# Optimization experiments

Measured on AMD Instinct MI355X. Metric: run time of the kernel, lower is better.

## Reference

```python
import jax, jax.numpy as jnp
import numpy as np

B, N, C = 4, 2048, 768
H = 12
HD = C // H

def setup_inputs() -> dict:
    key = jax.random.key(0)
    k1, k2, k3, k4, k5 = jax.random.split(key, 5)
    x = jax.random.normal(k1, (B, N, C), dtype=jnp.float32)
    qkv_w = jax.random.normal(k2, (3 * C, C), dtype=jnp.float32) * (1.0 / np.sqrt(C))
    qkv_b = jax.random.normal(k3, (3 * C,), dtype=jnp.float32) * 0.02
    proj_w = jax.random.normal(k4, (C, C), dtype=jnp.float32) * (1.0 / np.sqrt(C))
    proj_b = jax.random.normal(k5, (C,), dtype=jnp.float32) * 0.02
    return {"x": x, "qkv_w": qkv_w, "qkv_b": qkv_b, "proj_w": proj_w, "proj_b": proj_b}

def reference(x, qkv_w, qkv_b, proj_w, proj_b):
    scale = HD ** (-0.5)
    # qkv projection: (B,N,3C)
    qkv = x @ qkv_w.T + qkv_b
    qkv = qkv.reshape(B, N, 3, H, HD).transpose(2, 0, 3, 1, 4)  # (3,B,H,N,HD)
    q, k, v = qkv[0], qkv[1], qkv[2]
    attn = jnp.einsum('bhqd,bhkd->bhqk', q, k) * scale  # (B,H,N,N)
    mask_value = -jnp.finfo(attn.dtype).max
    causal_mask = jnp.triu(jnp.ones((N, N), dtype=bool), k=1)
    attn = jnp.where(causal_mask, mask_value, attn)
    attn = jax.nn.softmax(attn, axis=-1)
    out = jnp.einsum('bhqk,bhkd->bhqd', attn, v)  # (B,H,N,HD)
    out = out.transpose(0, 2, 1, 3).reshape(B, N, C)
    return out @ proj_w.T + proj_b
```

## Files before the change

### kernel.cpp

```cpp
#include <hip/hip_runtime.h>
#include <hip/hip_bf16.h>


typedef __attribute__((ext_vector_type(8))) short bf16x8;
typedef __attribute__((ext_vector_type(4))) float f32x4;
typedef __attribute__((ext_vector_type(16))) float f32x16;

typedef __attribute__((address_space(3))) unsigned int lds_uint;
typedef __attribute__((address_space(1))) const unsigned int gbl_uint;

__device__ __forceinline__ void gload16(const void* g, void* l) {
  __builtin_amdgcn_global_load_lds((gbl_uint*)g, (lds_uint*)l, 16, 0, 0);
}

__device__ __forceinline__ unsigned short f2bf(float f) {
  unsigned u = __float_as_uint(f);
  unsigned rounding = 0x7FFFu + ((u >> 16) & 1u);
  return (unsigned short)((u + rounding) >> 16);
}

__device__ __forceinline__ unsigned cvtpk(float lo, float hi) {
  unsigned r;
  asm("v_cvt_pk_bf16_f32 %0, %1, %2" : "=v"(r) : "v"(lo), "v"(hi));
  return r;
}

__device__ __forceinline__ float exp2a(float x) {
  float r;
  asm("v_exp_f32 %0, %1" : "=v"(r) : "v"(x));
  return r;
}

__global__ void cast_f32_to_bf16(const float* __restrict__ in,
                                 unsigned short* __restrict__ out, int n) {
  int idx = blockIdx.x * blockDim.x + threadIdx.x;
  int stride = gridDim.x * blockDim.x;
  for (int i = idx * 4; i < n; i += stride * 4) {
    float4 v = *reinterpret_cast<const float4*>(in + i);
    ushort4 o;
    o.x = f2bf(v.x); o.y = f2bf(v.y); o.z = f2bf(v.z); o.w = f2bf(v.w);
    *reinterpret_cast<ushort4*>(out + i) = o;
  }
}

template <bool OUT_F32>
__global__ __launch_bounds__(256) void gemm_bt_kernel(
    const unsigned short* __restrict__ A,
    const unsigned short* __restrict__ Bw,
    const float* __restrict__ bias,
    void* __restrict__ Cout,
    int M, int Ncols, int K, int ldc) {
  __shared__ __align__(16) short As[2][4096];
  __shared__ __align__(16) short Bs[2][4096];

  const int t = threadIdx.x;
  const int lane = t & 63;
  const int wave = t >> 6;
  const int wm = wave >> 1;
  const int wn = wave & 1;
  const int m0 = blockIdx.y * 128;
  const int n0 = blockIdx.x * 128;
  const int lrow = lane & 15;
  const int lk = (lane >> 4) * 8;

  const int srow = t >> 2, scol = (t & 3) * 8;
  const unsigned short* gA0 = A + (size_t)(m0 + srow) * K + scol;
  const unsigned short* gA1 = gA0 + (size_t)64 * K;
  const unsigned short* gB0 = Bw + (size_t)(n0 + srow) * K + scol;
  const unsigned short* gB1 = gB0 + (size_t)64 * K;
  const int db0 = wave * 512, db1 = 2048 + wave * 512;

  f32x4 acc[4][4] = {};
  const int nk = K / 32;

  gload16(gA0, &As[0][db0]); gload16(gA1, &As[0][db1]);
  gload16(gB0, &Bs[0][db0]); gload16(gB1, &Bs[0][db1]);

  int cur = 0;
  for (int kk = 0; kk < nk; ++kk) {
    __syncthreads();
    if (kk + 1 < nk) {
      const int off = (kk + 1) * 32;
      gload16(gA0 + off, &As[cur ^ 1][db0]); gload16(gA1 + off, &As[cur ^ 1][db1]);
      gload16(gB0 + off, &Bs[cur ^ 1][db0]); gload16(gB1 + off, &Bs[cur ^ 1][db1]);
    }
    bf16x8 a[4], b[4];
#pragma unroll
    for (int m = 0; m < 4; ++m)
      a[m] = *reinterpret_cast<const bf16x8*>(&As[cur][(wm * 64 + m * 16 + lrow) * 32 + lk]);
#pragma unroll
    for (int n = 0; n < 4; ++n)
      b[n] = *reinterpret_cast<const bf16x8*>(&Bs[cur][(wn * 64 + n * 16 + lrow) * 32 + lk]);
#pragma unroll
    for (int m = 0; m < 4; ++m)
#pragma unroll
      for (int n = 0; n < 4; ++n)
        acc[m][n] = __builtin_amdgcn_mfma_f32_16x16x32_bf16(a[m], b[n], acc[m][n], 0, 0, 0);
    cur ^= 1;
  }

  const int orow0 = (lane >> 4) * 4;
  const int ocol = lane & 15;
#pragma unroll
  for (int m = 0; m < 4; ++m) {
#pragma unroll
    for (int n = 0; n < 4; ++n) {
      const int c = n0 + wn * 64 + n * 16 + ocol;
      const float bv = bias[c];
#pragma unroll
      for (int r = 0; r < 4; ++r) {
        const int rr = m0 + wm * 64 + m * 16 + orow0 + r;
        const float v = acc[m][n][r] + bv;
        if (OUT_F32)
          reinterpret_cast<float*>(Cout)[(size_t)rr * ldc + c] = v;
        else
          reinterpret_cast<unsigned short*>(Cout)[(size_t)rr * ldc + c] = f2bf(v);
      }
    }
  }
}

#define ATT_N 2048
#define ATT_H 12
#define QKV_LD 2304

__global__ __launch_bounds__(256) void transpose_v(
    const unsigned short* __restrict__ qkv, unsigned short* __restrict__ vt) {
  const int kb = blockIdx.x;
  const int bh = blockIdx.y;
  const int t = threadIdx.x;
  const int b = bh / ATT_H, h = bh % ATT_H;
  const int d0 = (t & 7) * 8;
  const unsigned short* src = qkv + (size_t)(b * ATT_N) * QKV_LD + 1536 + h * 64 + d0;
  unsigned short* dst = vt + (size_t)bh * 64 * ATT_N + kb * 256;
#pragma unroll
  for (int kk = 0; kk < 8; ++kk) {
    const int ko = (t >> 3) + kk * 32;
    bf16x8 v = *reinterpret_cast<const bf16x8*>(src + (size_t)(kb * 256 + ko) * QKV_LD);
#pragma unroll
    for (int j = 0; j < 8; ++j)
      dst[(size_t)(d0 + j) * ATT_N + ko] = v[j];
  }
}

__global__ __launch_bounds__(256) void attn_kernel(
    const unsigned short* __restrict__ qkv,
    const unsigned short* __restrict__ vt,
    unsigned short* __restrict__ out) {
  __shared__ __align__(16) short Ks[2][4096];
  __shared__ __align__(16) short Vs[2][4096];

  const int t = threadIdx.x;
  const int lane = t & 63;
  const int w = t >> 6;
  const int hi = lane >> 5;
  const int l31 = lane & 31;

  const int wid = blockIdx.x;
  const int pj = wid / 48;
  const int bh = wid % 48;
  const int b = bh / ATT_H;
  const int h = bh % ATT_H;

  const size_t rowbase = (size_t)b * ATT_N;
  const unsigned short* qptr = qkv + rowbase * QKV_LD + h * 64;
  const unsigned short* kptr = qptr + 768;
  const unsigned short* vtptr = vt + (size_t)bh * 64 * ATT_N;

  int kKr[2], kKc[2];
#pragma unroll
  for (int c = 0; c < 2; ++c) {
    const int i = t + c * 256;
    const int f = i >> 6, ls = i & 63;
    kKr[c] = (f >> 2) * 32 + (ls & 31);
    kKc[c] = (f & 3) * 2 + (ls >> 5);
  }
  const unsigned short* gK0 = kptr + (size_t)kKr[0] * QKV_LD + kKc[0] * 8;
  const unsigned short* gK1 = kptr + (size_t)kKr[1] * QKV_LD + kKc[1] * 8;
  const unsigned short* gV0 = vtptr + (size_t)kKr[0] * ATT_N + kKc[0] * 8;
  const unsigned short* gV1 = vtptr + (size_t)kKr[1] * ATT_N + kKc[1] * 8;
  const int db0 = w * 512, db1 = 2048 + w * 512;

  for (int ph = 0; ph < 2; ++ph) {
    const int qb = ph ? pj : 15 - pj;
    const int q0w = qb * 128 + w * 32;
    const int qg = q0w + l31;
    const int nt = (qb + 1) * 2;

    bf16x8 qf[4];
#pragma unroll
    for (int dk = 0; dk < 4; ++dk)
      qf[dk] = *reinterpret_cast<const bf16x8*>(
          qptr + (size_t)(q0w + l31) * QKV_LD + dk * 16 + hi * 8);

    f32x16 O0 = {}, O1 = {};
    float lrun = 0.f;

    __syncthreads();
    gload16(gK0, &Ks[0][db0]); gload16(gK1, &Ks[0][db1]);
    gload16(gV0, &Vs[0][db0]); gload16(gV1, &Vs[0][db1]);

    int cur = 0;
    for (int kt = 0; kt < nt; ++kt) {
      const int k0 = kt * 64;
      __syncthreads();
      if (kt + 1 < nt) {
        const size_t advk = (size_t)(k0 + 64) * QKV_LD;
        gload16(gK0 + advk, &Ks[cur ^ 1][db0]); gload16(gK1 + advk, &Ks[cur ^ 1][db1]);
        gload16(gV0 + (k0 + 64), &Vs[cur ^ 1][db0]);
        gload16(gV1 + (k0 + 64), &Vs[cur ^ 1][db1]);
      }

      if (k0 <= q0w + 31) {
        f32x16 S0 = {}, S1 = {};
        __builtin_amdgcn_s_setprio(1);
#pragma unroll
        for (int dk = 0; dk < 4; ++dk) {
          bf16x8 kf = *reinterpret_cast<const bf16x8*>(&Ks[cur][(dk * 64 + lane) * 8]);
          S0 = __builtin_amdgcn_mfma_f32_32x32x16_bf16(kf, qf[dk], S0, 0, 0, 0);
        }
#pragma unroll
        for (int dk = 0; dk < 4; ++dk) {
          bf16x8 kf = *reinterpret_cast<const bf16x8*>(&Ks[cur][((4 + dk) * 64 + lane) * 8]);
          S1 = __builtin_amdgcn_mfma_f32_32x32x16_bf16(kf, qf[dk], S1, 0, 0, 0);
        }
        __builtin_amdgcn_s_setprio(0);

        const float scale2 = 0.18033688f;
        float p0[16], p1[16];
        if (k0 + 63 <= q0w) {
#pragma unroll
          for (int r = 0; r < 16; ++r) {
            p0[r] = exp2a(S0[r] * scale2);
            p1[r] = exp2a(S1[r] * scale2);
          }
        } else {
#pragma unroll
          for (int r = 0; r < 16; ++r) {
            int row = (r & 3) + 8 * (r >> 2) + 4 * hi;
            float e0 = (k0 + row > qg) ? -1e30f : S0[r] * scale2;
            float e1 = (k0 + 32 + row > qg) ? -1e30f : S1[r] * scale2;
            p0[r] = exp2a(e0);
            p1[r] = exp2a(e1);
          }
        }

        float sa = 0.f, sb = 0.f;
#pragma unroll
        for (int r = 0; r < 16; r += 2) { sa += p0[r] + p1[r]; sb += p0[r + 1] + p1[r + 1]; }
        float rsum = sa + sb;
        rsum += __shfl_xor(rsum, 32);
        lrun += rsum;

        bf16x8 Ub[4];
#pragma unroll
        for (int s = 0; s < 2; ++s) {
          unsigned pu[4][2];
#pragma unroll
          for (int m = 0; m < 4; ++m)
#pragma unroll
            for (int c = 0; c < 2; ++c)
              pu[m][c] = s ? cvtpk(p1[4 * m + 2 * c], p1[4 * m + 2 * c + 1])
                           : cvtpk(p0[4 * m + 2 * c], p0[4 * m + 2 * c + 1]);
#pragma unroll
          for (int tt = 0; tt < 2; ++tt) {
            unsigned s0v = hi ? pu[2 * tt][0] : pu[2 * tt + 1][0];
            unsigned s1v = hi ? pu[2 * tt][1] : pu[2 * tt + 1][1];
            unsigned r0 = __shfl_xor(s0v, 32);
            unsigned r1 = __shfl_xor(s1v, 32);
            union { unsigned u[4]; bf16x8 v; } U;
            U.u[0] = hi ? r0 : pu[2 * tt][0];
            U.u[1] = hi ? r1 : pu[2 * tt][1];
            U.u[2] = hi ? pu[2 * tt + 1][0] : r0;
            U.u[3] = hi ? pu[2 * tt + 1][1] : r1;
            Ub[s * 2 + tt] = U.v;
          }
        }

        __builtin_amdgcn_s_setprio(1);
#pragma unroll
        for (int ks = 0; ks < 4; ++ks) {
          bf16x8 vf0 = *reinterpret_cast<const bf16x8*>(&Vs[cur][(ks * 64 + lane) * 8]);
          O0 = __builtin_amdgcn_mfma_f32_32x32x16_bf16(vf0, Ub[ks], O0, 0, 0, 0);
          bf16x8 vf1 = *reinterpret_cast<const bf16x8*>(&Vs[cur][((4 + ks) * 64 + lane) * 8]);
          O1 = __builtin_amdgcn_mfma_f32_32x32x16_bf16(vf1, Ub[ks], O1, 0, 0, 0);
        }
        __builtin_amdgcn_s_setprio(0);
      }
      cur ^= 1;
    }

    const float inv = 1.0f / lrun;
    unsigned short* orow = out + (rowbase + q0w + l31) * 768 + h * 64;
#pragma unroll
    for (int half = 0; half < 2; ++half) {
      const f32x16& O = half ? O1 : O0;
#pragma unroll
      for (int m = 0; m < 4; ++m) {
        uint2 o2;
        o2.x = cvtpk(O[4 * m + 0] * inv, O[4 * m + 1] * inv);
        o2.y = cvtpk(O[4 * m + 2] * inv, O[4 * m + 3] * inv);
        *reinterpret_cast<uint2*>(orow + half * 32 + 8 * m + 4 * hi) = o2;
      }
    }
  }
}

extern "C" void kernel_launch(void* const* d_in, const int* in_sizes, int n_in,
                              void* d_out, int out_size, void* d_ws, size_t ws_size,
                              hipStream_t stream) {
  const float* x = (const float*)d_in[0];
  const float* qkv_w = (const float*)d_in[1];
  const float* qkv_b = (const float*)d_in[2];
  const float* proj_w = (const float*)d_in[3];
  const float* proj_b = (const float*)d_in[4];
  float* out = (float*)d_out;

  unsigned short* x_bf = (unsigned short*)d_ws;
  unsigned short* qw_bf = x_bf + (size_t)8192 * 768;
  unsigned short* pw_bf = qw_bf + (size_t)2304 * 768;
  unsigned short* qkv = pw_bf + (size_t)768 * 768;
  unsigned short* attno = qkv + (size_t)8192 * 2304;
  unsigned short* vtb = attno + (size_t)8192 * 768;

  cast_f32_to_bf16<<<dim3(1024), dim3(256), 0, stream>>>(x, x_bf, 8192 * 768);
  cast_f32_to_bf16<<<dim3(512), dim3(256), 0, stream>>>(qkv_w, qw_bf, 2304 * 768);
  cast_f32_to_bf16<<<dim3(256), dim3(256), 0, stream>>>(proj_w, pw_bf, 768 * 768);

  gemm_bt_kernel<false><<<dim3(18, 64), dim3(256), 0, stream>>>(
      x_bf, qw_bf, qkv_b, qkv, 8192, 2304, 768, 2304);
  transpose_v<<<dim3(8, 48), dim3(256), 0, stream>>>(qkv, vtb);
  attn_kernel<<<dim3(384), dim3(256), 0, stream>>>(qkv, vtb, attno);
  gemm_bt_kernel<true><<<dim3(6, 64), dim3(256), 0, stream>>>(
      attno, pw_bf, proj_b, out, 8192, 768, 768, 768);
}
```

Before: 163.8 us.

## Give each wave 64 query rows and drop the paired causal-block schedule

Each wave now handles 64 query rows in two 32-row groups instead of 32, so every K and V fragment read from LDS feeds two MFMAs. Work blocks become 256-query tiles processed largest-first (qb = 7 - wid/48), replacing the earlier scheme where each block handled two 128-row tiles paired for load balance. This roughly halves LDS traffic per unit of compute. In exchange it uses more registers (four accumulators, double the Q fragments), which can lower occupancy. Causal work per block is now uneven, and whether the grid launch was updated to match the new block count is not visible in the code shown.

```diff
diff --git a/kernel.cpp b/kernel.cpp
--- a/kernel.cpp
+++ b/kernel.cpp
@@ -157,7 +157,7 @@
   const int l31 = lane & 31;
 
   const int wid = blockIdx.x;
-  const int pj = wid / 48;
+  const int qb = 7 - (wid / 48);
   const int bh = wid % 48;
   const int b = bh / ATT_H;
   const int h = bh % ATT_H;
@@ -166,6 +166,21 @@
   const unsigned short* qptr = qkv + rowbase * QKV_LD + h * 64;
   const unsigned short* kptr = qptr + 768;
   const unsigned short* vtptr = vt + (size_t)bh * 64 * ATT_N;
+
+  const int q0w = qb * 256 + w * 64;
+  const int nt = (qb + 1) * 4;
+
+  bf16x8 qf0[4], qf1[4];
+#pragma unroll
+  for (int dk = 0; dk < 4; ++dk) {
+    qf0[dk] = *reinterpret_cast<const bf16x8*>(
+        qptr + (size_t)(q0w + l31) * QKV_LD + dk * 16 + hi * 8);
+    qf1[dk] = *reinterpret_cast<const bf16x8*>(
+        qptr + (size_t)(q0w + 32 + l31) * QKV_LD + dk * 16 + hi * 8);
+  }
+
+  f32x16 O00 = {}, O01 = {}, O10 = {}, O11 = {};
+  float lrun0 = 0.f, lrun1 = 0.f;
 
   int kKr[2], kKc[2];
 #pragma unroll
@@ -181,87 +196,72 @@
   const unsigned short* gV1 = vtptr + (size_t)kKr[1] * ATT_N + kKc[1] * 8;
   const int db0 = w * 512, db1 = 2048 + w * 512;
 
-  for (int ph = 0; ph < 2; ++ph) {
-    const int qb = ph ? pj : 15 - pj;
-    const int q0w = qb * 128 + w * 32;
-    const int qg = q0w + l31;
-    const int nt = (qb + 1) * 2;
-
-    bf16x8 qf[4];
-#pragma unroll
-    for (int dk = 0; dk < 4; ++dk)
-      qf[dk] = *reinterpret_cast<const bf16x8*>(
-          qptr + (size_t)(q0w + l31) * QKV_LD + dk * 16 + hi * 8);
-
-    f32x16 O0 = {}, O1 = {};
-    float lrun = 0.f;
-
+  gload16(gK0, &Ks[0][db0]); gload16(gK1, &Ks[0][db1]);
+  gload16(gV0, &Vs[0][db0]); gload16(gV1, &Vs[0][db1]);
+
+  int cur = 0;
+  for (int kt = 0; kt < nt; ++kt) {
+    const int k0 = kt * 64;
     __syncthreads();
-    gload16(gK0, &Ks[0][db0]); gload16(gK1, &Ks[0][db1]);
-    gload16(gV0, &Vs[0][db0]); gload16(gV1, &Vs[0][db1]);
-
-    int cur = 0;
-    for (int kt = 0; kt < nt; ++kt) {
-      const int k0 = kt * 64;
-      __syncthreads();
-      if (kt + 1 < nt) {
-        const size_t advk = (size_t)(k0 + 64) * QKV_LD;
-        gload16(gK0 + advk, &Ks[cur ^ 1][db0]); gload16(gK1 + advk, &Ks[cur ^ 1][db1]);
-        gload16(gV0 + (k0 + 64), &Vs[cur ^ 1][db0]);
-        gload16(gV1 + (k0 + 64), &Vs[cur ^ 1][db1]);
-      }
-
-      if (k0 <= q0w + 31) {
+    if (kt + 1 < nt) {
+      const size_t advk = (size_t)(k0 + 64) * QKV_LD;
+      gload16(gK0 + advk, &Ks[cur ^ 1][db0]); gload16(gK1 + advk, &Ks[cur ^ 1][db1]);
+      gload16(gV0 + (k0 + 64), &Vs[cur ^ 1][db0]);
+      gload16(gV1 + (k0 + 64), &Vs[cur ^ 1][db1]);
+    }
+
+    if (k0 <= q0w + 63) {
+#pragma unroll
+      for (int kh = 0; kh < 2; ++kh) {
+        const int kbase = k0 + kh * 32;
+        if (kbase > q0w + 63) break;
+
         f32x16 S0 = {}, S1 = {};
         __builtin_amdgcn_s_setprio(1);
 #pragma unroll
         for (int dk = 0; dk < 4; ++dk) {
-          bf16x8 kf = *reinterpret_cast<const bf16x8*>(&Ks[cur][(dk * 64 + lane) * 8]);
-          S0 = __builtin_amdgcn_mfma_f32_32x32x16_bf16(kf, qf[dk], S0, 0, 0, 0);
-        }
-#pragma unroll
-        for (int dk = 0; dk < 4; ++dk) {
-          bf16x8 kf = *reinterpret_cast<const bf16x8*>(&Ks[cur][((4 + dk) * 64 + lane) * 8]);
-          S1 = __builtin_amdgcn_mfma_f32_32x32x16_bf16(kf, qf[dk], S1, 0, 0, 0);
+          bf16x8 kf = *reinterpret_cast<const bf16x8*>(
+              &Ks[cur][((kh * 4 + dk) * 64 + lane) * 8]);
+          S0 = __builtin_amdgcn_mfma_f32_32x32x16_bf16(kf, qf0[dk], S0, 0, 0, 0);
+          S1 = __builtin_amdgcn_mfma_f32_32x32x16_bf16(kf, qf1[dk], S1, 0, 0, 0);
         }
         __builtin_amdgcn_s_setprio(0);
 
         const float scale2 = 0.18033688f;
         float p0[16], p1[16];
-        if (k0 + 63 <= q0w) {
+        if (kbase + 31 <= q0w) {
 #pragma unroll
           for (int r = 0; r < 16; ++r) {
             p0[r] = exp2a(S0[r] * scale2);
             p1[r] = exp2a(S1[r] * scale2);
           }
         } else {
+          const int qg0 = q0w + l31, qg1 = q0w + 32 + l31;
 #pragma unroll
           for (int r = 0; r < 16; ++r) {
-            int row = (r & 3) + 8 * (r >> 2) + 4 * hi;
-            float e0 = (k0 + row > qg) ? -1e30f : S0[r] * scale2;
-            float e1 = (k0 + 32 + row > qg) ? -1e30f : S1[r] * scale2;
-            p0[r] = exp2a(e0);
-            p1[r] = exp2a(e1);
+            const int key = kbase + (r & 3) + 8 * (r >> 2) + 4 * hi;
+            p0[r] = exp2a((key > qg0) ? -1e30f : S0[r] * scale2);
+            p1[r] = exp2a((key > qg1) ? -1e30f : S1[r] * scale2);
           }
         }
 
-        float sa = 0.f, sb = 0.f;
-#pragma unroll
-        for (int r = 0; r < 16; r += 2) { sa += p0[r] + p1[r]; sb += p0[r + 1] + p1[r + 1]; }
-        float rsum = sa + sb;
-        rsum += __shfl_xor(rsum, 32);
-        lrun += rsum;
-
-        bf16x8 Ub[4];
-#pragma unroll
-        for (int s = 0; s < 2; ++s) {
+        float ra = 0.f, rb = 0.f;
+#pragma unroll
+        for (int r = 0; r < 16; ++r) { ra += p0[r]; rb += p1[r]; }
+        ra += __shfl_xor(ra, 32);
+        rb += __shfl_xor(rb, 32);
+        lrun0 += ra; lrun1 += rb;
+
+        bf16x8 Ub0[2], Ub1[2];
+#pragma unroll
+        for (int g = 0; g < 2; ++g) {
+          const float* p = g ? p1 : p0;
           unsigned pu[4][2];
 #pragma unroll
           for (int m = 0; m < 4; ++m)
 #pragma unroll
             for (int c = 0; c < 2; ++c)
-              pu[m][c] = s ? cvtpk(p1[4 * m + 2 * c], p1[4 * m + 2 * c + 1])
-                           : cvtpk(p0[4 * m + 2 * c], p0[4 * m + 2 * c + 1]);
+              pu[m][c] = cvtpk(p[4 * m + 2 * c], p[4 * m + 2 * c + 1]);
 #pragma unroll
           for (int tt = 0; tt < 2; ++tt) {
             unsigned s0v = hi ? pu[2 * tt][0] : pu[2 * tt + 1][0];
@@ -273,34 +273,40 @@
             U.u[1] = hi ? r1 : pu[2 * tt][1];
             U.u[2] = hi ? pu[2 * tt + 1][0] : r0;
             U.u[3] = hi ? pu[2 * tt + 1][1] : r1;
-            Ub[s * 2 + tt] = U.v;
+            if (g == 0) Ub0[tt] = U.v; else Ub1[tt] = U.v;
           }
         }
 
         __builtin_amdgcn_s_setprio(1);
 #pragma unroll
-        for (int ks = 0; ks < 4; ++ks) {
+        for (int tt = 0; tt < 2; ++tt) {
+          const int ks = kh * 2 + tt;
           bf16x8 vf0 = *reinterpret_cast<const bf16x8*>(&Vs[cur][(ks * 64 + lane) * 8]);
-          O0 = __builtin_amdgcn_mfma_f32_32x32x16_bf16(vf0, Ub[ks], O0, 0, 0, 0);
+          O00 = __builtin_amdgcn_mfma_f32_32x32x16_bf16(vf0, Ub0[tt], O00, 0, 0, 0);
+          O01 = __builtin_amdgcn_mfma_f32_32x32x16_bf16(vf0, Ub1[tt], O01, 0, 0, 0);
           bf16x8 vf1 = *reinterpret_cast<const bf16x8*>(&Vs[cur][((4 + ks) * 64 + lane) * 8]);
-          O1 = __builtin_amdgcn_mfma_f32_32x32x16_bf16(vf1, Ub[ks], O1, 0, 0, 0);
+          O10 = __builtin_amdgcn_mfma_f32_32x32x16_bf16(vf1, Ub0[tt], O10, 0, 0, 0);
+          O11 = __builtin_amdgcn_mfma_f32_32x32x16_bf16(vf1, Ub1[tt], O11, 0, 0, 0);
         }
         __builtin_amdgcn_s_setprio(0);
       }
-      cur ^= 1;
-    }
-
-    const float inv = 1.0f / lrun;
-    unsigned short* orow = out + (rowbase + q0w + l31) * 768 + h * 64;
-#pragma unroll
-    for (int half = 0; half < 2; ++half) {
-      const f32x16& O = half ? O1 : O0;
+    }
+    cur ^= 1;
+  }
+
+#pragma unroll
+  for (int g = 0; g < 2; ++g) {
+    const float inv = 1.0f / (g ? lrun1 : lrun0);
+    unsigned short* orow = out + (rowbase + q0w + g * 32 + l31) * 768 + h * 64;
+#pragma unroll
+    for (int dh = 0; dh < 2; ++dh) {
+      const f32x16& O = g ? (dh ? O11 : O01) : (dh ? O10 : O00);
 #pragma unroll
       for (int m = 0; m < 4; ++m) {
         uint2 o2;
         o2.x = cvtpk(O[4 * m + 0] * inv, O[4 * m + 1] * inv);
         o2.y = cvtpk(O[4 * m + 2] * inv, O[4 * m + 3] * inv);
-        *reinterpret_cast<uint2*>(orow + half * 32 + 8 * m + 4 * hi) = o2;
+        *reinterpret_cast<uint2*>(orow + dh * 32 + 8 * m + 4 * hi) = o2;
       }
     }
   }
```

Result: slower. 186.4 us (+13.8%).
